# Kernel optimization log

Measured on AMD Instinct MI355X. Metric: run time of the kernel, lower is better.

Reference implementation:

```python
import jax, jax.numpy as jnp
import numpy as np

WS = 8   # window size
NH = 8   # num heads


def layernorm(x, g, b, eps=1e-5):
    m = jnp.mean(x, axis=-1, keepdims=True)
    v = jnp.var(x, axis=-1, keepdims=True)
    return (x - m) * jax.lax.rsqrt(v + eps) * g + b


def setup_inputs() -> dict:
    key = jax.random.key(0)
    ks = jax.random.split(key, 8)
    B, C, H, W = 16, 256, 64, 64
    s = 0.02
    inp = {
        "x": jax.random.normal(ks[0], (B, C, H, W), jnp.float32),
        "norm1_g": jnp.ones((C,), jnp.float32),
        "norm1_b": jnp.zeros((C,), jnp.float32),
        "qkv_w": jax.random.normal(ks[1], (3 * C, C), jnp.float32) * s,
        "qkv_b": jnp.zeros((3 * C,), jnp.float32),
        "rel_bias_table": jax.random.normal(ks[2], ((2 * WS - 1) ** 2, NH), jnp.float32) * s,
        "proj_w": jax.random.normal(ks[3], (C, C), jnp.float32) * s,
        "proj_b": jnp.zeros((C,), jnp.float32),
        "norm2_g": jnp.ones((C,), jnp.float32),
        "norm2_b": jnp.zeros((C,), jnp.float32),
        "fc1_w": jax.random.normal(ks[4], (4 * C, C), jnp.float32) * s,
        "fc1_b": jnp.zeros((4 * C,), jnp.float32),
        "fc2_w": jax.random.normal(ks[5], (C, 4 * C), jnp.float32) * s,
        "fc2_b": jnp.zeros((C,), jnp.float32),
    }
    # relative position index (Swin standard), shape (WS*WS, WS*WS), int constant
    coords = np.stack(np.meshgrid(np.arange(WS), np.arange(WS), indexing="ij")).reshape(2, -1)
    rel = (coords[:, :, None] - coords[:, None, :]).transpose(1, 2, 0)
    rel[:, :, 0] += WS - 1
    rel[:, :, 1] += WS - 1
    rel[:, :, 0] *= 2 * WS - 1
    inp["rel_index"] = jnp.asarray(rel.sum(-1), jnp.int32)
    return inp


def reference(x, norm1_g, norm1_b, qkv_w, qkv_b, rel_bias_table, proj_w, proj_b,
              norm2_g, norm2_b, fc1_w, fc1_b, fc2_w, fc2_b, rel_index):
    B, C, H, W = x.shape
    N = WS * WS
    hd = C // NH
    scale = hd ** -0.5

    xs = jnp.transpose(x, (0, 2, 3, 1)).reshape(B, H * W, C)  # b (h w) c
    shortcut = xs

    y = layernorm(xs, norm1_g, norm1_b).reshape(B, H, W, C)
    # window partition -> (B*nW, N, C); shift_size = 0 (default), no cyclic shift / mask
    y = y.reshape(B, H // WS, WS, W // WS, WS, C).transpose(0, 1, 3, 2, 4, 5).reshape(-1, N, C)

    qkv = (y @ qkv_w.T + qkv_b).reshape(-1, N, 3, NH, hd).transpose(2, 0, 3, 1, 4)
    q, k, v = qkv[0], qkv[1], qkv[2]  # each (nW*B, NH, N, hd)

    attn = jnp.einsum("whnd,whmd->whnm", q * scale, k)
    bias = rel_bias_table[rel_index].transpose(2, 0, 1)  # (NH, N, N)
    attn = jax.nn.softmax(attn + bias[None], axis=-1)
    out = jnp.einsum("whnm,whmd->whnd", attn, v).transpose(0, 2, 1, 3).reshape(-1, N, C)
    out = out @ proj_w.T + proj_b

    # window reverse -> (B, H*W, C)
    out = out.reshape(B, H // WS, W // WS, WS, WS, C).transpose(0, 1, 3, 2, 4, 5).reshape(B, H * W, C)

    xs = shortcut + out
    h = layernorm(xs, norm2_g, norm2_b)
    h = jax.nn.gelu(h @ fc1_w.T + fc1_b, approximate=False) @ fc2_w.T + fc2_b
    xs = xs + h

    return jnp.transpose(xs.reshape(B, H, W, C), (0, 3, 1, 2))
```

## Files before the change

### kernel.cpp

```cpp
#include <hip/hip_runtime.h>

typedef unsigned short u16;
typedef __attribute__((ext_vector_type(8))) short short8;
typedef __attribute__((ext_vector_type(4))) float f32x4;

#define MFMA16(a, b, c) __builtin_amdgcn_mfma_f32_16x16x32_bf16((a), (b), (c), 0, 0, 0)

__device__ __forceinline__ u16 f2b(float f) {
  unsigned b = __float_as_uint(f);
  b += 0x7FFFu + ((b >> 16) & 1u);
  return (u16)(b >> 16);
}

__device__ __forceinline__ void gload_lds16(const void* g, void* l) {
  __builtin_amdgcn_global_load_lds((const __attribute__((address_space(1))) void*)g,
                                   (__attribute__((address_space(3))) void*)l, 16, 0, 0);
}

__device__ __forceinline__ float fast_gelu(float x) {
  const float u = x * 0.70710678118654752f;
  const float au = fabsf(u);
  float d = 1.f + 0.3275911f * au;
  float tt;
  asm("v_rcp_f32 %0, %1" : "=v"(tt) : "v"(d));
  float p = 1.061405429f * tt - 1.453152027f;
  p = p * tt + 1.421413741f;
  p = p * tt - 0.284496736f;
  p = p * tt + 0.254829592f;
  p = p * tt;
  const float e = __expf(-u * u);
  const float erf_au = 1.f - p * e;
  return 0.5f * x * (1.f + copysignf(erf_au, x));
}

__global__ __launch_bounds__(256) void f2bf_kernel(const float* __restrict__ s,
                                                   u16* __restrict__ d, int n) {
  int i = blockIdx.x * 256 + threadIdx.x;
  if (i < n) d[i] = f2b(s[i]);
}

__global__ __launch_bounds__(256) void biasfull_kernel(const float* __restrict__ tbl,
                                                       const int* __restrict__ ridx,
                                                       float* __restrict__ o) {
  int i = blockIdx.x * 256 + threadIdx.x;
  int hm = i >> 12, nm = i & 4095;
  o[i] = tbl[ridx[nm] * 8 + hm];
}

__global__ __launch_bounds__(256) void ln1_win_kernel(const float* __restrict__ x,
                                                      const float* __restrict__ g,
                                                      const float* __restrict__ b,
                                                      u16* __restrict__ y) {
  __shared__ float red[2][4][64];
  const int bh = blockIdx.x;
  const int bb = bh >> 6, h = bh & 63;
  const int w = threadIdx.x & 63, cg = threadIdx.x >> 6;
  const float* xp = x + (size_t)bb * 1048576 + (size_t)h * 64 + w;
  float vals[64];
  float s = 0.f, ss = 0.f;
#pragma unroll
  for (int j = 0; j < 64; ++j) {
    float v = xp[(size_t)(cg * 64 + j) * 4096];
    vals[j] = v;
    s += v;
    ss += v * v;
  }
  red[0][cg][w] = s;
  red[1][cg][w] = ss;
  __syncthreads();
  const float S = red[0][0][w] + red[0][1][w] + red[0][2][w] + red[0][3][w];
  const float Q = red[1][0][w] + red[1][1][w] + red[1][2][w] + red[1][3][w];
  const float m = S * (1.f / 256.f);
  const float rstd = rsqrtf(Q * (1.f / 256.f) - m * m + 1e-5f);
  const int win = bb * 64 + ((h >> 3) << 3) + (w >> 3);
  const int tok = ((h & 7) << 3) + (w & 7);
  u16* yp = y + (size_t)win * 16384 + tok * 256 + cg * 64;
#pragma unroll
  for (int jj = 0; jj < 8; ++jj) {
    short8 o;
#pragma unroll
    for (int q = 0; q < 8; ++q) {
      const int c64 = jj * 8 + q;
      const int c = cg * 64 + c64;
      o[q] = (short)f2b((vals[c64] - m) * rstd * g[c] + b[c]);
    }
    *(short8*)&yp[jj * 8] = o;
  }
}

template <int EPI>
__global__ __launch_bounds__(256) void gemm_bt(const u16* __restrict__ A,
                                               const u16* __restrict__ W,
                                               const float* __restrict__ bias,
                                               u16* __restrict__ outh,
                                               float* __restrict__ outf,
                                               const float* __restrict__ aux,
                                               const int N, const int K) {
  __shared__ __align__(16) u16 As[2][128 * 64];
  __shared__ __align__(16) u16 Bs[2][128 * 64];
  const int ntiles = N >> 7;
  const int mt = blockIdx.x / ntiles;
  const int nt = blockIdx.x - mt * ntiles;
  const int tid = threadIdx.x;
  const int wv = tid >> 6, lane = tid & 63;
  const int wr = (wv >> 1) << 6;
  const int wc = (wv & 1) << 6;
  const int lrow = lane >> 3;
  const int lkswz = (((lane & 7) ^ (lane >> 3)) << 3);
  const int lr = lane & 15, lg = lane >> 4;
  const int swz = (lr & 7) << 3;
  f32x4 acc[4][4];
#pragma unroll
  for (int mi = 0; mi < 4; ++mi)
#pragma unroll
    for (int ni = 0; ni < 4; ++ni) acc[mi][ni] = (f32x4){0.f, 0.f, 0.f, 0.f};
  const u16* Ab = A + (size_t)mt * 128 * K;
  const u16* Wb = W + (size_t)nt * 128 * K;
  const int ntk = K >> 6;

  auto STAGE = [&](int bf, int t) {
    const int kt = t << 6;
#pragma unroll
    for (int i = 0; i < 4; ++i) {
      const int rb = wv * 32 + i * 8;
      gload_lds16(Ab + (size_t)(rb + lrow) * K + kt + lkswz, &As[bf][rb * 64]);
    }
#pragma unroll
    for (int i = 0; i < 4; ++i) {
      const int rb = wv * 32 + i * 8;
      gload_lds16(Wb + (size_t)(rb + lrow) * K + kt + lkswz, &Bs[bf][rb * 64]);
    }
  };

  STAGE(0, 0);
  __syncthreads();
  int cur = 0;
  for (int t = 0; t < ntk; ++t) {
    if (t + 1 < ntk) STAGE(cur ^ 1, t + 1);
#pragma unroll
    for (int kk = 0; kk < 2; ++kk) {
      const int kq = (kk * 32 + lg * 8) ^ swz;
      short8 a[4], bq[4];
#pragma unroll
      for (int mi = 0; mi < 4; ++mi)
        a[mi] = *(const short8*)&As[cur][(wr + mi * 16 + lr) * 64 + kq];
#pragma unroll
      for (int ni = 0; ni < 4; ++ni)
        bq[ni] = *(const short8*)&Bs[cur][(wc + ni * 16 + lr) * 64 + kq];
#pragma unroll
      for (int mi = 0; mi < 4; ++mi)
#pragma unroll
        for (int ni = 0; ni < 4; ++ni) acc[mi][ni] = MFMA16(a[mi], bq[ni], acc[mi][ni]);
    }
    __syncthreads();
    cur ^= 1;
  }
  const int row0 = mt * 128 + wr + lg * 4;
  const int col0 = nt * 128 + wc + lr;

  if constexpr (EPI == 0) {
#pragma unroll
    for (int mi = 0; mi < 4; ++mi)
#pragma unroll
      for (int ni = 0; ni < 4; ++ni) {
        const int col = col0 + ni * 16;
        const int which = col >> 8, cc = col & 255;
        const int head = cc >> 5, hd = cc & 31;
        u16* dst = outh + (size_t)which * 16777216ull;
        const float scl = (which == 0) ? 0.17677669529663689f : 1.0f;
        const float bv = bias[col];
#pragma unroll
        for (int r = 0; r < 4; ++r) {
          const int row = row0 + mi * 16 + r;
          const int win = row >> 6, tk = row & 63;
          dst[(((size_t)(win * 8 + head) << 6) + tk) * 32 + hd] =
              f2b((acc[mi][ni][r] + bv) * scl);
        }
      }
  } else if constexpr (EPI == 1) {
#pragma unroll
    for (int mi = 0; mi < 4; ++mi)
#pragma unroll
      for (int ni = 0; ni < 4; ++ni) {
        const int col = col0 + ni * 16;
        const float bv = bias[col];
#pragma unroll
        for (int r = 0; r < 4; ++r) {
          const int row = row0 + mi * 16 + r;
          const int win = row >> 6, tk = row & 63;
          const int bb = win >> 6;
          const int h = (((win >> 3) & 7) << 3) + (tk >> 3);
          const int w = ((win & 7) << 3) + (tk & 7);
          float val = acc[mi][ni][r] + bv +
                      aux[(((size_t)bb * 256 + col) * 64 + h) * 64 + w];
          outf[(size_t)row * 256 + col] = val;
        }
      }
  } else if constexpr (EPI == 2) {
#pragma unroll
    for (int mi = 0; mi < 4; ++mi)
#pragma unroll
      for (int ni = 0; ni < 4; ++ni) {
        const int col = col0 + ni * 16;
        const float bv = bias[col];
#pragma unroll
        for (int r = 0; r < 4; ++r) {
          const int row = row0 + mi * 16 + r;
          outh[(size_t)row * N + col] = f2b(fast_gelu(acc[mi][ni][r] + bv));
        }
      }
  } else {
#pragma unroll
    for (int mi = 0; mi < 4; ++mi)
#pragma unroll
      for (int ni = 0; ni < 4; ++ni) {
        const int col = col0 + ni * 16;
        const float bv = bias[col];
        const int row = row0 + mi * 16;
        const int win = row >> 6, tk = row & 63;
        const int bb = win >> 6;
        const int h = (((win >> 3) & 7) << 3) + (tk >> 3);
        const int w = ((win & 7) << 3) + (tk & 7);
        f32x4 v;
#pragma unroll
        for (int r = 0; r < 4; ++r)
          v[r] = acc[mi][ni][r] + bv + aux[(size_t)(row + r) * 256 + col];
        *(f32x4*)&outf[(((size_t)bb * 256 + col) * 64 + h) * 64 + w] = v;
      }
  }
}

__global__ __launch_bounds__(64) void attn_kernel(const u16* __restrict__ qkv,
                                                  const float* __restrict__ biasf,
                                                  u16* __restrict__ aout) {
  __shared__ __align__(16) u16 qs[64 * 40];
  __shared__ __align__(16) u16 ks[64 * 40];
  __shared__ __align__(16) u16 vt[32 * 72];
  __shared__ __align__(16) u16 pp[64 * 72];
  const int wh = blockIdx.x;
  const int head = wh & 7;
  const int win = wh >> 3;
  const int lane = threadIdx.x;
  const int lr = lane & 15, lg = lane >> 4;
  const u16* qg = qkv + (size_t)wh * 2048;
  const u16* kg = qkv + 16777216ull + (size_t)wh * 2048;
  const u16* vg = qkv + 33554432ull + (size_t)wh * 2048;
#pragma unroll
  for (int i = 0; i < 4; ++i) {
    int ch = i * 64 + lane;
    int r = ch >> 2, qo = (ch & 3) * 8;
    *(short8*)&qs[r * 40 + qo] = *(const short8*)&qg[r * 32 + qo];
    *(short8*)&ks[r * 40 + qo] = *(const short8*)&kg[r * 32 + qo];
  }
  {
    short8 v0 = *(const short8*)&vg[(size_t)lane * 32];
    short8 v1 = *(const short8*)&vg[(size_t)lane * 32 + 8];
    short8 v2 = *(const short8*)&vg[(size_t)lane * 32 + 16];
    short8 v3 = *(const short8*)&vg[(size_t)lane * 32 + 24];
#pragma unroll
    for (int j = 0; j < 8; ++j) {
      vt[j * 72 + lane] = (u16)v0[j];
      vt[(8 + j) * 72 + lane] = (u16)v1[j];
      vt[(16 + j) * 72 + lane] = (u16)v2[j];
      vt[(24 + j) * 72 + lane] = (u16)v3[j];
    }
  }
  __syncthreads();
  f32x4 sf[4][4];
#pragma unroll
  for (int mi = 0; mi < 4; ++mi)
#pragma unroll
    for (int ni = 0; ni < 4; ++ni) sf[mi][ni] = (f32x4){0.f, 0.f, 0.f, 0.f};
  {
    short8 a[4], bq[4];
#pragma unroll
    for (int mi = 0; mi < 4; ++mi) a[mi] = *(const short8*)&qs[(mi * 16 + lr) * 40 + lg * 8];
#pragma unroll
    for (int ni = 0; ni < 4; ++ni) bq[ni] = *(const short8*)&ks[(ni * 16 + lr) * 40 + lg * 8];
#pragma unroll
    for (int mi = 0; mi < 4; ++mi)
#pragma unroll
      for (int ni = 0; ni < 4; ++ni) sf[mi][ni] = MFMA16(a[mi], bq[ni], sf[mi][ni]);
  }
  const float* bh = biasf + (size_t)head * 4096;
#pragma unroll
  for (int mi = 0; mi < 4; ++mi) {
#pragma unroll
    for (int r = 0; r < 4; ++r) {
      const int n = mi * 16 + lg * 4 + r;
      float v0 = sf[mi][0][r] + bh[n * 64 + lr];
      float v1 = sf[mi][1][r] + bh[n * 64 + 16 + lr];
      float v2 = sf[mi][2][r] + bh[n * 64 + 32 + lr];
      float v3 = sf[mi][3][r] + bh[n * 64 + 48 + lr];
      float mx = fmaxf(fmaxf(v0, v1), fmaxf(v2, v3));
      mx = fmaxf(mx, __shfl_xor(mx, 1));
      mx = fmaxf(mx, __shfl_xor(mx, 2));
      mx = fmaxf(mx, __shfl_xor(mx, 4));
      mx = fmaxf(mx, __shfl_xor(mx, 8));
      float e0 = __expf(v0 - mx), e1 = __expf(v1 - mx);
      float e2 = __expf(v2 - mx), e3 = __expf(v3 - mx);
      float sm = e0 + e1 + e2 + e3;
      sm += __shfl_xor(sm, 1);
      sm += __shfl_xor(sm, 2);
      sm += __shfl_xor(sm, 4);
      sm += __shfl_xor(sm, 8);
      const float inv = 1.f / sm;
      pp[n * 72 + lr] = f2b(e0 * inv);
      pp[n * 72 + 16 + lr] = f2b(e1 * inv);
      pp[n * 72 + 32 + lr] = f2b(e2 * inv);
      pp[n * 72 + 48 + lr] = f2b(e3 * inv);
    }
  }
  __syncthreads();
  f32x4 o[4][2];
#pragma unroll
  for (int mi = 0; mi < 4; ++mi)
#pragma unroll
    for (int ni = 0; ni < 2; ++ni) o[mi][ni] = (f32x4){0.f, 0.f, 0.f, 0.f};
#pragma unroll
  for (int kk = 0; kk < 2; ++kk) {
    short8 pa[4], vb[2];
#pragma unroll
    for (int mi = 0; mi < 4; ++mi)
      pa[mi] = *(const short8*)&pp[(mi * 16 + lr) * 72 + kk * 32 + lg * 8];
#pragma unroll
    for (int ni = 0; ni < 2; ++ni)
      vb[ni] = *(const short8*)&vt[(ni * 16 + lr) * 72 + kk * 32 + lg * 8];
#pragma unroll
    for (int mi = 0; mi < 4; ++mi)
#pragma unroll
      for (int ni = 0; ni < 2; ++ni) o[mi][ni] = MFMA16(pa[mi], vb[ni], o[mi][ni]);
  }
  u16* op = aout + (size_t)win * 16384 + head * 32;
#pragma unroll
  for (int mi = 0; mi < 4; ++mi)
#pragma unroll
    for (int ni = 0; ni < 2; ++ni)
#pragma unroll
      for (int r = 0; r < 4; ++r) {
        const int n = mi * 16 + lg * 4 + r;
        op[(size_t)n * 256 + ni * 16 + lr] = f2b(o[mi][ni][r]);
      }
}

__global__ __launch_bounds__(256) void ln2_kernel(const float* __restrict__ xs2,
                                                  const float* __restrict__ g,
                                                  const float* __restrict__ b,
                                                  u16* __restrict__ h2) {
  const int wv = threadIdx.x >> 6, lane = threadIdx.x & 63;
  const size_t row = (size_t)blockIdx.x * 4 + wv;
  const f32x4 xv = *(const f32x4*)&xs2[row * 256 + lane * 4];
  float s = xv[0] + xv[1] + xv[2] + xv[3];
  float q = xv[0] * xv[0] + xv[1] * xv[1] + xv[2] * xv[2] + xv[3] * xv[3];
#pragma unroll
  for (int off = 1; off < 64; off <<= 1) {
    s += __shfl_xor(s, off);
    q += __shfl_xor(q, off);
  }
  const float m = s * (1.f / 256.f);
  const float rstd = rsqrtf(q * (1.f / 256.f) - m * m + 1e-5f);
  const f32x4 gv = *(const f32x4*)&g[lane * 4];
  const f32x4 bv = *(const f32x4*)&b[lane * 4];
  union {
    u16 u[4];
    unsigned long long v;
  } pk;
#pragma unroll
  for (int j = 0; j < 4; ++j) pk.u[j] = f2b((xv[j] - m) * rstd * gv[j] + bv[j]);
  *(unsigned long long*)&h2[row * 256 + lane * 4] = pk.v;
}

extern "C" void kernel_launch(void* const* d_in, const int* in_sizes, int n_in,
                              void* d_out, int out_size, void* d_ws, size_t ws_size,
                              hipStream_t stream) {
  const float* x = (const float*)d_in[0];
  const float* n1g = (const float*)d_in[1];
  const float* n1b = (const float*)d_in[2];
  const float* qkv_w = (const float*)d_in[3];
  const float* qkv_b = (const float*)d_in[4];
  const float* tbl = (const float*)d_in[5];
  const float* proj_w = (const float*)d_in[6];
  const float* proj_b = (const float*)d_in[7];
  const float* n2g = (const float*)d_in[8];
  const float* n2b = (const float*)d_in[9];
  const float* fc1_w = (const float*)d_in[10];
  const float* fc1_b = (const float*)d_in[11];
  const float* fc2_w = (const float*)d_in[12];
  const float* fc2_b = (const float*)d_in[13];
  const int* relidx = (const int*)d_in[14];
  float* outp = (float*)d_out;

  char* w = (char*)d_ws;
  const size_t Mi = 1ull << 20;
  if (ws_size < 237 * Mi) return;
  u16* Y = (u16*)(w + 0);
  u16* qb = (u16*)(w + 32 * Mi);
  u16* aout = (u16*)(w + 0);
  float* xs2 = (float*)(w + 32 * Mi);
  u16* h2 = (u16*)(w + 0);
  u16* h1 = (u16*)(w + 96 * Mi);
  u16* wqkv = (u16*)(w + 224 * Mi);
  u16* wproj = wqkv + 196608;
  u16* wfc1 = wproj + 65536;
  u16* wfc2 = wfc1 + 262144;
  float* bfull = (float*)(w + 224 * Mi + 1572864);

  f2bf_kernel<<<768, 256, 0, stream>>>(qkv_w, wqkv, 196608);
  f2bf_kernel<<<256, 256, 0, stream>>>(proj_w, wproj, 65536);
  f2bf_kernel<<<1024, 256, 0, stream>>>(fc1_w, wfc1, 262144);
  f2bf_kernel<<<1024, 256, 0, stream>>>(fc2_w, wfc2, 262144);
  biasfull_kernel<<<128, 256, 0, stream>>>(tbl, relidx, bfull);

  ln1_win_kernel<<<1024, 256, 0, stream>>>(x, n1g, n1b, Y);
  gemm_bt<0><<<512 * 6, 256, 0, stream>>>(Y, wqkv, qkv_b, qb, nullptr, nullptr, 768, 256);
  attn_kernel<<<8192, 64, 0, stream>>>(qb, bfull, aout);
  gemm_bt<1><<<512 * 2, 256, 0, stream>>>(aout, wproj, proj_b, nullptr, xs2, x, 256, 256);
  ln2_kernel<<<16384, 256, 0, stream>>>(xs2, n2g, n2b, h2);
  gemm_bt<2><<<512 * 8, 256, 0, stream>>>(h2, wfc1, fc1_b, h1, nullptr, nullptr, 1024, 256);
  gemm_bt<3><<<512 * 2, 256, 0, stream>>>(h1, wfc2, fc2_b, nullptr, outp, xs2, 256, 1024);
}
```

Measured before the change: 373.7 us.

## Prefetch two GEMM stages, remap blocks per XCD, fuse prep kernels, shrink attention LDS

The GEMM now uses compile-time K and N-tile counts with a fully unrolled loop. It prefetches two k-tiles ahead using explicit vmcnt waits and raw barriers, and declares launch bounds for two blocks per CU. Block indices are remapped so that each XCD handles a contiguous range of M tiles, which is meant to improve L2 reuse of A rows. The five weight and bias preprocessing kernels are merged into one launch to cut launch overhead. The attention kernel reuses the Q/K shared-memory region for the P matrix, with an added barrier, to lower LDS use and allow more resident blocks.

```diff
diff --git a/kernel.cpp b/kernel.cpp
--- a/kernel.cpp
+++ b/kernel.cpp
@@ -5,6 +5,9 @@
 typedef __attribute__((ext_vector_type(4))) float f32x4;
 
 #define MFMA16(a, b, c) __builtin_amdgcn_mfma_f32_16x16x32_bf16((a), (b), (c), 0, 0, 0)
+#define WAITV(N) asm volatile("s_waitcnt vmcnt(" #N ")" ::: "memory")
+#define BARS() __builtin_amdgcn_s_barrier()
+#define MFENCE() asm volatile("" ::: "memory")
 
 __device__ __forceinline__ u16 f2b(float f) {
   unsigned b = __float_as_uint(f);
@@ -33,18 +36,26 @@
   return 0.5f * x * (1.f + copysignf(erf_au, x));
 }
 
-__global__ __launch_bounds__(256) void f2bf_kernel(const float* __restrict__ s,
-                                                   u16* __restrict__ d, int n) {
+__global__ __launch_bounds__(256) void prep_kernel(
+    const float* __restrict__ qkv_w, const float* __restrict__ proj_w,
+    const float* __restrict__ fc1_w, const float* __restrict__ fc2_w,
+    const float* __restrict__ tbl, const int* __restrict__ ridx,
+    u16* __restrict__ wqkv, u16* __restrict__ wproj, u16* __restrict__ wfc1,
+    u16* __restrict__ wfc2, float* __restrict__ bfull) {
   int i = blockIdx.x * 256 + threadIdx.x;
-  if (i < n) d[i] = f2b(s[i]);
-}
-
-__global__ __launch_bounds__(256) void biasfull_kernel(const float* __restrict__ tbl,
-                                                       const int* __restrict__ ridx,
-                                                       float* __restrict__ o) {
-  int i = blockIdx.x * 256 + threadIdx.x;
-  int hm = i >> 12, nm = i & 4095;
-  o[i] = tbl[ridx[nm] * 8 + hm];
+  if (i < 196608) {
+    wqkv[i] = f2b(qkv_w[i]);
+  } else if (i < 262144) {
+    wproj[i - 196608] = f2b(proj_w[i - 196608]);
+  } else if (i < 524288) {
+    wfc1[i - 262144] = f2b(fc1_w[i - 262144]);
+  } else if (i < 786432) {
+    wfc2[i - 524288] = f2b(fc2_w[i - 524288]);
+  } else {
+    int j = i - 786432;
+    int hm = j >> 12, nm = j & 4095;
+    bfull[j] = tbl[ridx[nm] * 8 + hm];
+  }
 }
 
 __global__ __launch_bounds__(256) void ln1_win_kernel(const float* __restrict__ x,
@@ -88,25 +99,26 @@
   }
 }
 
-template <int EPI>
-__global__ __launch_bounds__(256) void gemm_bt(const u16* __restrict__ A,
-                                               const u16* __restrict__ W,
-                                               const float* __restrict__ bias,
-                                               u16* __restrict__ outh,
-                                               float* __restrict__ outf,
-                                               const float* __restrict__ aux,
-                                               const int N, const int K) {
-  __shared__ __align__(16) u16 As[2][128 * 64];
-  __shared__ __align__(16) u16 Bs[2][128 * 64];
-  const int ntiles = N >> 7;
-  const int mt = blockIdx.x / ntiles;
-  const int nt = blockIdx.x - mt * ntiles;
+template <int EPI, int KT, int NNT>
+__global__ __launch_bounds__(256, 2) void gemm_bt(const u16* __restrict__ A,
+                                                  const u16* __restrict__ W,
+                                                  const float* __restrict__ bias,
+                                                  u16* __restrict__ outh,
+                                                  float* __restrict__ outf,
+                                                  const float* __restrict__ aux) {
+  constexpr int NTK = KT >> 6;
+  constexpr int NC = NNT * 128;
+  __shared__ __align__(16) u16 As[2][8192];
+  __shared__ __align__(16) u16 Bs[2][8192];
+  const int xcd = blockIdx.x & 7, ii = blockIdx.x >> 3;
+  const int mt = xcd * 64 + ii / NNT;
+  const int nt = ii % NNT;
   const int tid = threadIdx.x;
   const int wv = tid >> 6, lane = tid & 63;
   const int wr = (wv >> 1) << 6;
   const int wc = (wv & 1) << 6;
   const int lrow = lane >> 3;
-  const int lkswz = (((lane & 7) ^ (lane >> 3)) << 3);
+  const int lkswz = (((lane & 7) ^ lrow) << 3);
   const int lr = lane & 15, lg = lane >> 4;
   const int swz = (lr & 7) << 3;
   f32x4 acc[4][4];
@@ -114,47 +126,55 @@
   for (int mi = 0; mi < 4; ++mi)
 #pragma unroll
     for (int ni = 0; ni < 4; ++ni) acc[mi][ni] = (f32x4){0.f, 0.f, 0.f, 0.f};
-  const u16* Ab = A + (size_t)mt * 128 * K;
-  const u16* Wb = W + (size_t)nt * 128 * K;
-  const int ntk = K >> 6;
-
-  auto STAGE = [&](int bf, int t) {
-    const int kt = t << 6;
-#pragma unroll
-    for (int i = 0; i < 4; ++i) {
-      const int rb = wv * 32 + i * 8;
-      gload_lds16(Ab + (size_t)(rb + lrow) * K + kt + lkswz, &As[bf][rb * 64]);
+  const u16* Ab = A + (size_t)mt * 128 * KT;
+  const u16* Wb = W + (size_t)nt * 128 * KT;
+
+#define STG(BF, T)                                                                      \
+  {                                                                                     \
+    const int kt_ = (T) << 6;                                                           \
+    _Pragma("unroll") for (int i_ = 0; i_ < 4; ++i_) {                                  \
+      const int rb_ = wv * 32 + i_ * 8;                                                 \
+      gload_lds16(Ab + (size_t)(rb_ + lrow) * KT + kt_ + lkswz, &As[BF][rb_ * 64]);     \
+    }                                                                                   \
+    _Pragma("unroll") for (int i_ = 0; i_ < 4; ++i_) {                                  \
+      const int rb_ = wv * 32 + i_ * 8;                                                 \
+      gload_lds16(Wb + (size_t)(rb_ + lrow) * KT + kt_ + lkswz, &Bs[BF][rb_ * 64]);     \
+    }                                                                                   \
+  }
+#define CMPT(BF)                                                                        \
+  {                                                                                     \
+    _Pragma("unroll") for (int kk = 0; kk < 2; ++kk) {                                  \
+      const int kq = (kk * 32 + lg * 8) ^ swz;                                          \
+      short8 a_[4], b_[4];                                                              \
+      _Pragma("unroll") for (int mi = 0; mi < 4; ++mi)                                  \
+          a_[mi] = *(const short8*)&As[BF][(wr + mi * 16 + lr) * 64 + kq];              \
+      _Pragma("unroll") for (int ni = 0; ni < 4; ++ni)                                  \
+          b_[ni] = *(const short8*)&Bs[BF][(wc + ni * 16 + lr) * 64 + kq];              \
+      _Pragma("unroll") for (int mi = 0; mi < 4; ++mi)                                  \
+          _Pragma("unroll") for (int ni = 0; ni < 4; ++ni)                              \
+              acc[mi][ni] = MFMA16(a_[mi], b_[ni], acc[mi][ni]);                        \
+    }                                                                                   \
+  }
+
+  STG(0, 0);
+  STG(1, 1);
+#pragma unroll
+  for (int t = 0; t < NTK; ++t) {
+    if (t + 1 < NTK) {
+      WAITV(8);
+    } else {
+      WAITV(0);
     }
-#pragma unroll
-    for (int i = 0; i < 4; ++i) {
-      const int rb = wv * 32 + i * 8;
-      gload_lds16(Wb + (size_t)(rb + lrow) * K + kt + lkswz, &Bs[bf][rb * 64]);
-    }
-  };
-
-  STAGE(0, 0);
-  __syncthreads();
-  int cur = 0;
-  for (int t = 0; t < ntk; ++t) {
-    if (t + 1 < ntk) STAGE(cur ^ 1, t + 1);
-#pragma unroll
-    for (int kk = 0; kk < 2; ++kk) {
-      const int kq = (kk * 32 + lg * 8) ^ swz;
-      short8 a[4], bq[4];
-#pragma unroll
-      for (int mi = 0; mi < 4; ++mi)
-        a[mi] = *(const short8*)&As[cur][(wr + mi * 16 + lr) * 64 + kq];
-#pragma unroll
-      for (int ni = 0; ni < 4; ++ni)
-        bq[ni] = *(const short8*)&Bs[cur][(wc + ni * 16 + lr) * 64 + kq];
-#pragma unroll
-      for (int mi = 0; mi < 4; ++mi)
-#pragma unroll
-        for (int ni = 0; ni < 4; ++ni) acc[mi][ni] = MFMA16(a[mi], bq[ni], acc[mi][ni]);
-    }
-    __syncthreads();
-    cur ^= 1;
-  }
+    BARS();
+    MFENCE();
+    CMPT(t & 1);
+    MFENCE();
+    BARS();
+    if (t + 2 < NTK) STG(t & 1, t + 2);
+  }
+#undef STG
+#undef CMPT
+
   const int row0 = mt * 128 + wr + lg * 4;
   const int col0 = nt * 128 + wc + lr;
 
@@ -206,7 +226,7 @@
 #pragma unroll
         for (int r = 0; r < 4; ++r) {
           const int row = row0 + mi * 16 + r;
-          outh[(size_t)row * N + col] = f2b(fast_gelu(acc[mi][ni][r] + bv));
+          outh[(size_t)row * NC + col] = f2b(fast_gelu(acc[mi][ni][r] + bv));
         }
       }
   } else {
@@ -233,10 +253,11 @@
 __global__ __launch_bounds__(64) void attn_kernel(const u16* __restrict__ qkv,
                                                   const float* __restrict__ biasf,
                                                   u16* __restrict__ aout) {
-  __shared__ __align__(16) u16 qs[64 * 40];
-  __shared__ __align__(16) u16 ks[64 * 40];
-  __shared__ __align__(16) u16 vt[32 * 72];
-  __shared__ __align__(16) u16 pp[64 * 72];
+  __shared__ __align__(16) u16 sqk[5120];
+  __shared__ __align__(16) u16 vt[2304];
+  u16* qs = sqk;
+  u16* ks = sqk + 2560;
+  u16* pp = sqk;
   const int wh = blockIdx.x;
   const int head = wh & 7;
   const int win = wh >> 3;
@@ -282,6 +303,7 @@
 #pragma unroll
       for (int ni = 0; ni < 4; ++ni) sf[mi][ni] = MFMA16(a[mi], bq[ni], sf[mi][ni]);
   }
+  __syncthreads();
   const float* bh = biasf + (size_t)head * 4096;
 #pragma unroll
   for (int mi = 0; mi < 4; ++mi) {
@@ -405,17 +427,13 @@
   u16* wfc2 = wfc1 + 262144;
   float* bfull = (float*)(w + 224 * Mi + 1572864);
 
-  f2bf_kernel<<<768, 256, 0, stream>>>(qkv_w, wqkv, 196608);
-  f2bf_kernel<<<256, 256, 0, stream>>>(proj_w, wproj, 65536);
-  f2bf_kernel<<<1024, 256, 0, stream>>>(fc1_w, wfc1, 262144);
-  f2bf_kernel<<<1024, 256, 0, stream>>>(fc2_w, wfc2, 262144);
-  biasfull_kernel<<<128, 256, 0, stream>>>(tbl, relidx, bfull);
-
+  prep_kernel<<<3200, 256, 0, stream>>>(qkv_w, proj_w, fc1_w, fc2_w, tbl, relidx, wqkv,
+                                        wproj, wfc1, wfc2, bfull);
   ln1_win_kernel<<<1024, 256, 0, stream>>>(x, n1g, n1b, Y);
-  gemm_bt<0><<<512 * 6, 256, 0, stream>>>(Y, wqkv, qkv_b, qb, nullptr, nullptr, 768, 256);
+  gemm_bt<0, 256, 6><<<3072, 256, 0, stream>>>(Y, wqkv, qkv_b, qb, nullptr, nullptr);
   attn_kernel<<<8192, 64, 0, stream>>>(qb, bfull, aout);
-  gemm_bt<1><<<512 * 2, 256, 0, stream>>>(aout, wproj, proj_b, nullptr, xs2, x, 256, 256);
+  gemm_bt<1, 256, 2><<<1024, 256, 0, stream>>>(aout, wproj, proj_b, nullptr, xs2, x);
   ln2_kernel<<<16384, 256, 0, stream>>>(xs2, n2g, n2b, h2);
-  gemm_bt<2><<<512 * 8, 256, 0, stream>>>(h2, wfc1, fc1_b, h1, nullptr, nullptr, 1024, 256);
-  gemm_bt<3><<<512 * 2, 256, 0, stream>>>(h1, wfc2, fc2_b, nullptr, outp, xs2, 256, 1024);
-}
+  gemm_bt<2, 256, 8><<<4096, 256, 0, stream>>>(h2, wfc1, fc1_b, h1, nullptr, nullptr);
+  gemm_bt<3, 1024, 2><<<1024, 256, 0, stream>>>(h1, wfc2, fc2_b, nullptr, outp, xs2);
+}
```

Result: faster. 300.1 us (-19.7%).
